# Kernel tuning notes

Hardware: AMD Instinct MI355X
Metric: run time of the kernel (lower is better)

The kernel has to match this reference:

```python
import jax, jax.numpy as jnp
import numpy as np

N, D_IN, H, OUT, L = 6144, 512, 512, 256, 3
EPS = 1e-5


def setup_inputs() -> dict:
    key = jax.random.key(0)
    ks = jax.random.split(key, 32)
    inp = {}
    inp["X"] = jax.random.normal(ks[0], (N, D_IN), dtype=jnp.float32)
    inp["adj"] = jax.random.randint(ks[1], (N, N), 0, 2).astype(jnp.float32)
    inp["adj_glo"] = jax.random.randint(ks[2], (N, N), 0, 2).astype(jnp.float32)
    s = 1.0 / np.sqrt(H)
    # projection + its BN
    inp["Wp"] = jax.random.normal(ks[3], (H, D_IN), dtype=jnp.float32) / np.sqrt(D_IN)
    inp["bp"] = jnp.zeros((H,), jnp.float32)
    inp["gp"] = jnp.ones((H,), jnp.float32)
    inp["betap"] = jnp.zeros((H,), jnp.float32)
    # per-layer params; layers 0,1 output H, layer 2 outputs OUT
    outs = [H, H, OUT]
    for i in range(L):
        o = outs[i]
        k = jax.random.split(ks[4 + i], 6)
        inp[f"Wq{i}"] = jax.random.normal(k[0], (H, H), jnp.float32) * s
        inp[f"Wk{i}"] = jax.random.normal(k[1], (H, H), jnp.float32) * s
        inp[f"Wv{i}"] = jax.random.normal(k[2], (H, H), jnp.float32) * s
        inp[f"Wo{i}"] = jax.random.normal(k[3], (o, H), jnp.float32) * s
        inp[f"bo{i}"] = jnp.zeros((o,), jnp.float32)
        inp[f"g{i}"] = jnp.ones((o,), jnp.float32)
        inp[f"beta{i}"] = jnp.zeros((o,), jnp.float32)
    return inp


def _normalize_adj(a):
    # symmetric GCN normalization D^{-1/2} A D^{-1/2}
    d = a.sum(axis=1)
    dis = jnp.where(d > 0, jax.lax.rsqrt(jnp.maximum(d, 1e-12)), 0.0)
    return a * dis[:, None] * dis[None, :]


def _bn(x, g, b):
    # BatchNorm1d, training mode: batch stats, biased variance
    m = x.mean(axis=0)
    v = x.var(axis=0)
    return g * (x - m) * jax.lax.rsqrt(v + EPS) + b


def _attn(h, adj, Wq, Wk, Wv, Wo, bo):
    Q = h @ Wq.T
    K = h @ Wk.T
    V = h @ Wv.T
    scores = (Q @ K.T) / np.sqrt(H)            # [N, N]
    scores = jnp.where(adj == 0, -jnp.inf, scores)
    attn = jax.nn.softmax(scores, axis=-1)
    return (attn @ V) @ Wo.T + bo


def reference(X, adj, adj_glo, Wp, bp, gp, betap,
              Wq0, Wk0, Wv0, Wo0, bo0, g0, beta0,
              Wq1, Wk1, Wv1, Wo1, bo1, g1, beta1,
              Wq2, Wk2, Wv2, Wo2, bo2, g2, beta2):
    # embedding: normalized global adjacency aggregation + projection + BN
    h = _normalize_adj(adj_glo) @ X
    h = h @ Wp.T + bp
    h = _bn(h, gp, betap)
    embed_features = h
    layers = [
        (Wq0, Wk0, Wv0, Wo0, bo0, g0, beta0),
        (Wq1, Wk1, Wv1, Wo1, bo1, g1, beta1),
        (Wq2, Wk2, Wv2, Wo2, bo2, g2, beta2),
    ]
    for i, (Wq, Wk, Wv, Wo, bo, g, b) in enumerate(layers):
        h_s = h
        h = _attn(h, adj, Wq, Wk, Wv, Wo, bo)
        h = jax.nn.relu(_bn(h, g, b))
        if i != L - 1:
            h = h + h_s
    return h, embed_features
```

## Files before the change

kernel.cpp:

```cpp
#include <hip/hip_runtime.h>
#include <cstdint>

#define NROW 6144
#define HDIM 512
#define DOUT 256
#define NEG_INF (-__builtin_inff())

typedef _Float16 half8 __attribute__((ext_vector_type(8)));
typedef _Float16 half4v __attribute__((ext_vector_type(4)));
typedef float f32x4 __attribute__((ext_vector_type(4)));

#define BARRIER() asm volatile("s_barrier" ::: "memory")
#define LGKM0()   asm volatile("s_waitcnt lgkmcnt(0)" ::: "memory")
#define VMCNT4()  asm volatile("s_waitcnt vmcnt(4)" ::: "memory")
#define VMCNT0()  asm volatile("s_waitcnt vmcnt(0)" ::: "memory")

__device__ __forceinline__ void gld_lds16(void* lds, const void* g) {
  __builtin_amdgcn_global_load_lds(
      (const __attribute__((address_space(1))) void*)g,
      (__attribute__((address_space(3))) void*)lds, 16, 0, 0);
}

__global__ __launch_bounds__(512, 2)
void gemm256(const _Float16* __restrict__ A, int lda,
             const _Float16* __restrict__ B, int ldb,
             _Float16* __restrict__ C, int ldc, int Kc, long MN)
{
  __shared__ _Float16 As[2][256][64];
  __shared__ _Float16 Bs[2][256][64];
  const int tid = threadIdx.x;
  const int wave = tid >> 6, lane = tid & 63;
  const int wr = wave >> 2, wc = wave & 3;

  const int gx = gridDim.x, gy = gridDim.y;
  const int nwg = gx * gy * gridDim.z;
  int lin = (blockIdx.z * gy + blockIdx.y) * gx + blockIdx.x;
  int swz = (nwg % 8 == 0) ? ((lin % 8) * (nwg >> 3) + (lin >> 3)) : lin;
  const int bx = swz % gx, by = (swz / gx) % gy, bz = swz / (gx * gy);
  const int row0 = bx * 256, col0 = by * 256;
  const _Float16* Ab = A + (size_t)row0 * lda + (size_t)bz * Kc;
  const _Float16* Bb = B + (size_t)col0 * ldb + (size_t)bz * Kc;
  const int nt = Kc >> 6;

  const int srow = lane >> 3;
  const int sgr  = (lane & 7) ^ srow;

  auto stageA = [&](int buf, int h, int t) {
    const _Float16* src = Ab + (size_t)(h * 128 + wave * 8 + srow) * lda + t * 64 + sgr * 8;
    gld_lds16(&As[buf][h * 128 + wave * 8][0], src);
    gld_lds16(&As[buf][h * 128 + 64 + wave * 8][0], src + (size_t)64 * lda);
  };
  auto stageB = [&](int buf, int h, int t) {
    const _Float16* src = Bb + (size_t)(h * 128 + wave * 8 + srow) * ldb + t * 64 + sgr * 8;
    gld_lds16(&Bs[buf][h * 128 + wave * 8][0], src);
    gld_lds16(&Bs[buf][h * 128 + 64 + wave * 8][0], src + (size_t)64 * ldb);
  };

  const int fr = lane & 15, sq = lane >> 4, fx = fr & 7;
  half8 af[4][2], bLo[2][2], bHi[2][2];
  f32x4 acc[8][4];
  const f32x4 vzero = {0.f, 0.f, 0.f, 0.f};
  #pragma unroll
  for (int f = 0; f < 8; ++f)
    #pragma unroll
    for (int j = 0; j < 4; ++j)
      acc[f][j] = vzero;

  auto dsA = [&](int buf, int mh) {
    #pragma unroll
    for (int i = 0; i < 4; ++i)
      #pragma unroll
      for (int ks = 0; ks < 2; ++ks)
        af[i][ks] = *(const half8*)&As[buf][wr * 128 + mh * 64 + i * 16 + fr]
                                          [((ks * 4 + sq) ^ fx) * 8];
  };
  auto dsBlo = [&](int buf) {
    #pragma unroll
    for (int jj = 0; jj < 2; ++jj)
      #pragma unroll
      for (int ks = 0; ks < 2; ++ks)
        bLo[jj][ks] = *(const half8*)&Bs[buf][wc * 64 + jj * 16 + fr]
                                            [((ks * 4 + sq) ^ fx) * 8];
  };
  auto dsBhi = [&](int buf) {
    #pragma unroll
    for (int jj = 0; jj < 2; ++jj)
      #pragma unroll
      for (int ks = 0; ks < 2; ++ks)
        bHi[jj][ks] = *(const half8*)&Bs[buf][wc * 64 + 32 + jj * 16 + fr]
                                            [((ks * 4 + sq) ^ fx) * 8];
  };
  auto mQlo = [&](int fb) {
    __builtin_amdgcn_s_setprio(1);
    #pragma unroll
    for (int i = 0; i < 4; ++i)
      #pragma unroll
      for (int jj = 0; jj < 2; ++jj)
        #pragma unroll
        for (int ks = 0; ks < 2; ++ks)
          acc[fb + i][jj] = __builtin_amdgcn_mfma_f32_16x16x32_f16(
              af[i][ks], bLo[jj][ks], acc[fb + i][jj], 0, 0, 0);
    __builtin_amdgcn_s_setprio(0);
  };
  auto mQhi = [&](int fb) {
    __builtin_amdgcn_s_setprio(1);
    #pragma unroll
    for (int i = 0; i < 4; ++i)
      #pragma unroll
      for (int jj = 0; jj < 2; ++jj)
        #pragma unroll
        for (int ks = 0; ks < 2; ++ks)
          acc[fb + i][2 + jj] = __builtin_amdgcn_mfma_f32_16x16x32_f16(
              af[i][ks], bHi[jj][ks], acc[fb + i][2 + jj], 0, 0, 0);
    __builtin_amdgcn_s_setprio(0);
  };

  stageA(0, 0, 0); stageA(0, 1, 0); stageB(0, 0, 0); stageB(0, 1, 0);
  stageB(1, 0, 1); stageB(1, 1, 1);
  VMCNT4();
  BARRIER();

  for (int T = 0; T < nt; T += 2) {
    const bool pipe = (T + 2 < nt);
    dsA(0, 0); dsBlo(0);
    stageA(1, 0, T + 1);
    BARRIER(); LGKM0(); mQlo(0); BARRIER();
    dsBhi(0);
    stageA(1, 1, T + 1);
    BARRIER(); LGKM0(); mQhi(0); BARRIER();
    dsA(0, 1);
    if (pipe) stageB(0, 0, T + 2);
    BARRIER(); LGKM0(); mQhi(4); BARRIER();
    if (pipe) { stageB(0, 1, T + 2); VMCNT4(); } else { VMCNT0(); }
    BARRIER(); mQlo(4); BARRIER();
    dsA(1, 0); dsBlo(1);
    if (pipe) stageA(0, 0, T + 2);
    BARRIER(); LGKM0(); mQlo(0); BARRIER();
    dsBhi(1);
    if (pipe) stageA(0, 1, T + 2);
    BARRIER(); LGKM0(); mQhi(0); BARRIER();
    dsA(1, 1);
    if (pipe) stageB(1, 0, T + 3);
    BARRIER(); LGKM0(); mQhi(4); BARRIER();
    if (pipe) { stageB(1, 1, T + 3); VMCNT4(); } else { VMCNT0(); }
    BARRIER(); mQlo(4); BARRIER();
  }

  _Float16* dst = C + (size_t)bz * MN;
  #pragma unroll
  for (int f = 0; f < 8; ++f)
    #pragma unroll
    for (int j = 0; j < 4; ++j)
      #pragma unroll
      for (int r = 0; r < 4; ++r) {
        int row = row0 + wr * 128 + f * 16 + sq * 4 + r;
        int col = col0 + wc * 64 + j * 16 + fr;
        dst[(size_t)row * ldc + col] = (_Float16)acc[f][j][r];
      }
}

__global__ __launch_bounds__(256)
void gemm_f16(const _Float16* __restrict__ A, int lda,
              const _Float16* __restrict__ B, int ldb,
              float* __restrict__ Cf, _Float16* __restrict__ Ch, int ldc,
              int Kc, _Float16* __restrict__ Pk, long MN)
{
  __shared__ _Float16 As[128][32];
  __shared__ _Float16 Bs[128][32];
  const int tid = threadIdx.x;
  const int wave = tid >> 6, lane = tid & 63;
  const int wr = wave >> 1, wc = wave & 1;
  const int row0 = blockIdx.x * 128, col0 = blockIdx.y * 128;
  const int kbase = blockIdx.z * Kc;

  const int sr = lane >> 2;
  const int sk = ((lane & 3) ^ ((lane >> 3) & 3)) * 8;

  f32x4 acc[4][4];
  const f32x4 vzero = {0.f, 0.f, 0.f, 0.f};
  #pragma unroll
  for (int i = 0; i < 4; ++i)
    #pragma unroll
    for (int j = 0; j < 4; ++j)
      acc[i][j] = vzero;

  const int fr = lane & 15;
  const int fk = (((lane >> 4) ^ ((fr >> 1) & 3))) * 8;

  for (int k0 = kbase; k0 < kbase + Kc; k0 += 32) {
    #pragma unroll
    for (int c = 0; c < 2; ++c) {
      int rbase = c * 64 + wave * 16;
      gld_lds16(&As[rbase][0], A + (size_t)(row0 + rbase + sr) * lda + k0 + sk);
      gld_lds16(&Bs[rbase][0], B + (size_t)(col0 + rbase + sr) * ldb + k0 + sk);
    }
    __syncthreads();
    half8 af[4], bf[4];
    #pragma unroll
    for (int i = 0; i < 4; ++i)
      af[i] = *(const half8*)&As[wr * 64 + i * 16 + fr][fk];
    #pragma unroll
    for (int j = 0; j < 4; ++j)
      bf[j] = *(const half8*)&Bs[wc * 64 + j * 16 + fr][fk];
    #pragma unroll
    for (int i = 0; i < 4; ++i)
      #pragma unroll
      for (int j = 0; j < 4; ++j)
        acc[i][j] = __builtin_amdgcn_mfma_f32_16x16x32_f16(af[i], bf[j], acc[i][j], 0, 0, 0);
    __syncthreads();
  }

  const int lr = (lane >> 4) * 4;
  const int lc = lane & 15;
  if (Pk) {
    _Float16* dst = Pk + (size_t)blockIdx.z * MN;
    #pragma unroll
    for (int i = 0; i < 4; ++i)
      #pragma unroll
      for (int j = 0; j < 4; ++j)
        #pragma unroll
        for (int r = 0; r < 4; ++r) {
          int row = row0 + wr * 64 + i * 16 + lr + r;
          int col = col0 + wc * 64 + j * 16 + lc;
          dst[(size_t)row * ldc + col] = (_Float16)acc[i][j][r];
        }
    return;
  }
  #pragma unroll
  for (int i = 0; i < 4; ++i)
    #pragma unroll
    for (int j = 0; j < 4; ++j)
      #pragma unroll
      for (int r = 0; r < 4; ++r) {
        int row = row0 + wr * 64 + i * 16 + lr + r;
        int col = col0 + wc * 64 + j * 16 + lc;
        float v = acc[i][j][r];
        if (Cf) Cf[(size_t)row * ldc + col] = v;
        if (Ch) Ch[(size_t)row * ldc + col] = (_Float16)v;
      }
}

__global__ __launch_bounds__(256)
void reduce_splitk(const _Float16* __restrict__ Pk, long MN, int S, int cshift,
                   const float* __restrict__ rowscale,
                   float* __restrict__ Yf, _Float16* __restrict__ Yh)
{
  long n4 = MN >> 2;
  for (long i = (long)blockIdx.x * 256 + threadIdx.x; i < n4; i += (long)gridDim.x * 256) {
    float s0 = 0, s1 = 0, s2 = 0, s3 = 0;
    for (int z = 0; z < S; ++z) {
      half4v p = ((const half4v*)(Pk + (size_t)z * MN))[i];
      s0 += (float)p[0]; s1 += (float)p[1]; s2 += (float)p[2]; s3 += (float)p[3];
    }
    if (rowscale) {
      float sc = rowscale[(i * 4) >> cshift];
      s0 *= sc; s1 *= sc; s2 *= sc; s3 *= sc;
    }
    if (Yf) {
      float4 o; o.x = s0; o.y = s1; o.z = s2; o.w = s3;
      ((float4*)Yf)[i] = o;
    }
    if (Yh) {
      half4v o;
      o[0] = (_Float16)s0; o[1] = (_Float16)s1; o[2] = (_Float16)s2; o[3] = (_Float16)s3;
      ((half4v*)Yh)[i] = o;
    }
  }
}

__global__ __launch_bounds__(256)
void degree_convert(const float* __restrict__ A, _Float16* __restrict__ Ah,
                    float* __restrict__ dis)
{
  const int row = blockIdx.x;
  const float* a = A + (size_t)row * NROW;
  _Float16* o = Ah + (size_t)row * NROW;
  float s = 0.f;
  #pragma unroll
  for (int it = 0; it < 6; ++it) {
    int j = it * 1024 + threadIdx.x * 4;
    float4 v = *(const float4*)&a[j];
    s += v.x + v.y + v.z + v.w;
    half4v h;
    h[0] = (_Float16)v.x; h[1] = (_Float16)v.y; h[2] = (_Float16)v.z; h[3] = (_Float16)v.w;
    *(half4v*)&o[j] = h;
  }
  #pragma unroll
  for (int off = 32; off; off >>= 1) s += __shfl_xor(s, off);
  __shared__ float red[4];
  if ((threadIdx.x & 63) == 0) red[threadIdx.x >> 6] = s;
  __syncthreads();
  if (threadIdx.x == 0) {
    float d = red[0] + red[1] + red[2] + red[3];
    dis[row] = (d > 0.f) ? rsqrtf(fmaxf(d, 1e-12f)) : 0.f;
  }
}

__global__ __launch_bounds__(192)
void build_mask(const float* __restrict__ adj, uint32_t* __restrict__ bits)
{
  const int row = blockIdx.x;
  const int w = threadIdx.x;
  const float* a = adj + (size_t)row * NROW + w * 32;
  uint32_t m = 0;
  #pragma unroll
  for (int q = 0; q < 8; ++q) {
    float4 x = *(const float4*)&a[q * 4];
    m |= (x.x != 0.f ? 1u : 0u) << (q * 4 + 0);
    m |= (x.y != 0.f ? 1u : 0u) << (q * 4 + 1);
    m |= (x.z != 0.f ? 1u : 0u) << (q * 4 + 2);
    m |= (x.w != 0.f ? 1u : 0u) << (q * 4 + 3);
  }
  bits[(size_t)row * 192 + w] = m;
}

__global__ __launch_bounds__(256)
void convert_f16(const float* __restrict__ x, _Float16* __restrict__ y, float scale, long n4)
{
  for (long i = (long)blockIdx.x * 256 + threadIdx.x; i < n4; i += (long)gridDim.x * 256) {
    float4 v = ((const float4*)x)[i];
    half4v o;
    o[0] = (_Float16)(v.x * scale);
    o[1] = (_Float16)(v.y * scale);
    o[2] = (_Float16)(v.z * scale);
    o[3] = (_Float16)(v.w * scale);
    ((half4v*)y)[i] = o;
  }
}

__global__ __launch_bounds__(256)
void transpose_scale_f16(const float* __restrict__ src, const float* __restrict__ rowscale,
                         _Float16* __restrict__ dst, int R, int C)
{
  __shared__ _Float16 tile[64][72];
  const int c0 = blockIdx.x * 64, r0 = blockIdx.y * 64;
  const int tx4 = (threadIdx.x & 15) * 4, ty = threadIdx.x >> 4;
  #pragma unroll
  for (int p = 0; p < 4; ++p) {
    int r = p * 16 + ty;
    float4 v = *(const float4*)&src[(size_t)(r0 + r) * C + c0 + tx4];
    float sc = rowscale ? rowscale[r0 + r] : 1.0f;
    tile[tx4 + 0][r] = (_Float16)(v.x * sc);
    tile[tx4 + 1][r] = (_Float16)(v.y * sc);
    tile[tx4 + 2][r] = (_Float16)(v.z * sc);
    tile[tx4 + 3][r] = (_Float16)(v.w * sc);
  }
  __syncthreads();
  #pragma unroll
  for (int p = 0; p < 4; ++p) {
    int c = p * 16 + ty;
    half4v o;
    o[0] = tile[c][tx4 + 0];
    o[1] = tile[c][tx4 + 1];
    o[2] = tile[c][tx4 + 2];
    o[3] = tile[c][tx4 + 3];
    *(half4v*)&dst[(size_t)(c0 + c) * R + r0 + tx4] = o;
  }
}

__global__ __launch_bounds__(256)
void transpose_f16(const _Float16* __restrict__ src, int ld,
                   _Float16* __restrict__ dst, int R, int C)
{
  __shared__ _Float16 tile[64][72];
  const int c0 = blockIdx.x * 64, r0 = blockIdx.y * 64;
  const int tx4 = (threadIdx.x & 15) * 4, ty = threadIdx.x >> 4;
  #pragma unroll
  for (int p = 0; p < 4; ++p) {
    int r = p * 16 + ty;
    half4v v = *(const half4v*)&src[(size_t)(r0 + r) * ld + c0 + tx4];
    tile[tx4 + 0][r] = v[0];
    tile[tx4 + 1][r] = v[1];
    tile[tx4 + 2][r] = v[2];
    tile[tx4 + 3][r] = v[3];
  }
  __syncthreads();
  #pragma unroll
  for (int p = 0; p < 4; ++p) {
    int c = p * 16 + ty;
    half4v o;
    o[0] = tile[c][tx4 + 0];
    o[1] = tile[c][tx4 + 1];
    o[2] = tile[c][tx4 + 2];
    o[3] = tile[c][tx4 + 3];
    *(half4v*)&dst[(size_t)(c0 + c) * R + r0 + tx4] = o;
  }
}

__global__ __launch_bounds__(256)
void softmax_mask16(_Float16* __restrict__ Sf, const uint32_t* __restrict__ bits,
                    float* __restrict__ linv)
{
  const int row = blockIdx.x;
  _Float16* s = Sf + (size_t)row * NROW;
  const uint32_t* b = bits + (size_t)row * 192;
  const int tid = threadIdx.x;
  float v[24];
  float m = NEG_INF;
  #pragma unroll
  for (int it = 0; it < 3; ++it) {
    int j = it * 2048 + tid * 8;
    half8 sv = *(const half8*)&s[j];
    uint32_t w = (b[j >> 5] >> (j & 31)) & 0xffu;
    #pragma unroll
    for (int e = 0; e < 8; ++e) {
      float x = ((w >> e) & 1u) ? (float)sv[e] : NEG_INF;
      v[it * 8 + e] = x;
      m = fmaxf(m, x);
    }
  }
  #pragma unroll
  for (int off = 32; off; off >>= 1) m = fmaxf(m, __shfl_xor(m, off));
  __shared__ float red[4];
  const int lane = tid & 63, wave = tid >> 6;
  if (lane == 0) red[wave] = m;
  __syncthreads();
  m = fmaxf(fmaxf(red[0], red[1]), fmaxf(red[2], red[3]));
  __syncthreads();
  float l = 0.f;
  #pragma unroll
  for (int k = 0; k < 24; ++k) {
    float e = (v[k] == NEG_INF) ? 0.f : __expf(v[k] - m);
    v[k] = e; l += e;
  }
  #pragma unroll
  for (int off = 32; off; off >>= 1) l += __shfl_xor(l, off);
  if (lane == 0) red[wave] = l;
  __syncthreads();
  l = red[0] + red[1] + red[2] + red[3];
  if (tid == 0) linv[row] = (l > 0.f) ? (1.f / l) : 0.f;
  #pragma unroll
  for (int it = 0; it < 3; ++it) {
    int j = it * 2048 + tid * 8;
    half8 o;
    #pragma unroll
    for (int e = 0; e < 8; ++e) o[e] = (_Float16)v[it * 8 + e];
    *(half8*)&s[j] = o;
  }
}

__global__ __launch_bounds__(256)
void bn_partial(const _Float16* __restrict__ X, int C,
                float* __restrict__ psum, float* __restrict__ psq)
{
  const int b = blockIdx.x;
  const int tid = threadIdx.x;
  const _Float16* x = X + (size_t)b * 128 * C;
  float s0 = 0, q0 = 0, s1 = 0, q1 = 0;
  for (int r = 0; r < 128; ++r) {
    float a = (float)x[(size_t)r * C + tid];
    s0 += a; q0 += a * a;
    if (C == 512) {
      float c2 = (float)x[(size_t)r * C + tid + 256];
      s1 += c2; q1 += c2 * c2;
    }
  }
  psum[b * C + tid] = s0; psq[b * C + tid] = q0;
  if (C == 512) { psum[b * C + tid + 256] = s1; psq[b * C + tid + 256] = q1; }
}

__global__ void bn_finalize(const float* __restrict__ psum, const float* __restrict__ psq,
                            int C, const float* __restrict__ g, const float* __restrict__ beta,
                            float* __restrict__ scale, float* __restrict__ shift)
{
  int c = threadIdx.x + blockIdx.x * blockDim.x;
  if (c >= C) return;
  float s = 0, q = 0;
  for (int b = 0; b < 48; ++b) { s += psum[b * C + c]; q += psq[b * C + c]; }
  const float invN = 1.0f / 6144.0f;
  float mean = s * invN;
  float var = q * invN - mean * mean;
  float rstd = rsqrtf(fmaxf(var, 0.f) + 1e-5f);
  float sc = g[c] * rstd;
  scale[c] = sc;
  shift[c] = beta[c] - mean * sc;
}

__global__ __launch_bounds__(256)
void bn_apply(const _Float16* __restrict__ X, const float* __restrict__ scale,
              const float* __restrict__ shift, const _Float16* __restrict__ residual,
              float* __restrict__ Yf, _Float16* __restrict__ Yh,
              int Cmask, long total, int do_relu)
{
  for (long i = (long)blockIdx.x * 256 + threadIdx.x; i < total; i += (long)gridDim.x * 256) {
    int c = (int)(i & Cmask);
    float v = (float)X[i] * scale[c] + shift[c];
    if (do_relu) v = fmaxf(v, 0.f);
    if (residual) v += (float)residual[i];
    if (Yf) Yf[i] = v;
    if (Yh) Yh[i] = (_Float16)v;
  }
}

extern "C" void kernel_launch(void* const* d_in, const int* in_sizes, int n_in,
                              void* d_out, int out_size, void* d_ws, size_t ws_size,
                              hipStream_t stream)
{
  (void)in_sizes; (void)n_in; (void)out_size; (void)ws_size;
  const float* X     = (const float*)d_in[0];
  const float* adj   = (const float*)d_in[1];
  const float* adjg  = (const float*)d_in[2];
  const float* Wp    = (const float*)d_in[3];
  const float* gp    = (const float*)d_in[5];
  const float* betap = (const float*)d_in[6];

  float* out_h     = (float*)d_out;
  float* out_embed = out_h + (size_t)NROW * DOUT;

  char* base = (char*)d_ws;
  size_t off = 0;
  auto alloc = [&](size_t bytes) -> void* {
    void* p = base + off;
    off += (bytes + 255) & ~(size_t)255;
    return p;
  };

  const long MN512 = (long)NROW * 512;

  _Float16* Ag  = (_Float16*)alloc((size_t)NROW * NROW * 2);
  _Float16* Sf  = Ag;
  uint32_t* bits = (uint32_t*)alloc((size_t)NROW * 192 * 4);
  _Float16* Pk  = (_Float16*)alloc((size_t)16 * MN512 * 2);
  _Float16* XsT = (_Float16*)alloc((size_t)HDIM * NROW * 2);
  _Float16* Yh16 = (_Float16*)alloc((size_t)NROW * HDIM * 2);
  _Float16* Wph = (_Float16*)alloc((size_t)HDIM * HDIM * 2);
  _Float16* QKVW[3];
  for (int i = 0; i < 3; ++i) QKVW[i] = (_Float16*)alloc((size_t)1536 * HDIM * 2);
  _Float16* Woh[3];
  Woh[0] = (_Float16*)alloc((size_t)512 * 512 * 2);
  Woh[1] = (_Float16*)alloc((size_t)512 * 512 * 2);
  Woh[2] = (_Float16*)alloc((size_t)256 * 512 * 2);
  _Float16* QKVh = (_Float16*)alloc((size_t)NROW * 1536 * 2);
  _Float16* VTh  = (_Float16*)alloc((size_t)HDIM * NROW * 2);
  _Float16* AVh  = (_Float16*)alloc((size_t)NROW * HDIM * 2);
  _Float16* xh   = (_Float16*)alloc((size_t)NROW * HDIM * 2);
  _Float16* hb16A = (_Float16*)alloc((size_t)NROW * HDIM * 2);
  _Float16* hb16B = (_Float16*)alloc((size_t)NROW * HDIM * 2);
  float* dis  = (float*)alloc((size_t)NROW * 4);
  float* linv = (float*)alloc((size_t)NROW * 4);
  float* psum = (float*)alloc((size_t)48 * 512 * 4);
  float* psq  = (float*)alloc((size_t)48 * 512 * 4);
  float* bnsc = (float*)alloc(512 * 4);
  float* bnsh = (float*)alloc(512 * 4);

  const float qk_scale = 0.21022410381342863f;

  degree_convert<<<NROW, 256, 0, stream>>>(adjg, Ag, dis);
  build_mask<<<NROW, 192, 0, stream>>>(adj, bits);
  transpose_scale_f16<<<dim3(8, 96), 256, 0, stream>>>(X, dis, XsT, NROW, HDIM);
  convert_f16<<<128, 256, 0, stream>>>(Wp, Wph, 1.f, 512 * 512 / 4);
  for (int i = 0; i < 3; ++i) {
    const float* Wq = (const float*)d_in[7 + i * 7 + 0];
    const float* Wk = (const float*)d_in[7 + i * 7 + 1];
    const float* Wv = (const float*)d_in[7 + i * 7 + 2];
    const float* Wo = (const float*)d_in[7 + i * 7 + 3];
    int o = (i < 2) ? 512 : 256;
    convert_f16<<<128, 256, 0, stream>>>(Wq, QKVW[i], qk_scale, 512 * 512 / 4);
    convert_f16<<<128, 256, 0, stream>>>(Wk, QKVW[i] + 512 * 512, qk_scale, 512 * 512 / 4);
    convert_f16<<<128, 256, 0, stream>>>(Wv, QKVW[i] + 2 * 512 * 512, 1.f, 512 * 512 / 4);
    convert_f16<<<128, 256, 0, stream>>>(Wo, Woh[i], 1.f, (long)o * 512 / 4);
  }

  gemm256<<<dim3(24, 2, 16), 512, 0, stream>>>(Ag, NROW, XsT, NROW, Pk, 512, 384, MN512);
  reduce_splitk<<<1536, 256, 0, stream>>>(Pk, MN512, 16, 9, dis, nullptr, Yh16);
  gemm_f16<<<dim3(48, 4), 256, 0, stream>>>(Yh16, HDIM, Wph, HDIM, nullptr, xh, HDIM,
                                            512, nullptr, 0);
  bn_partial<<<48, 256, 0, stream>>>(xh, 512, psum, psq);
  bn_finalize<<<2, 256, 0, stream>>>(psum, psq, 512, gp, betap, bnsc, bnsh);
  bn_apply<<<2048, 256, 0, stream>>>(xh, bnsc, bnsh, nullptr, out_embed, hb16A,
                                     511, MN512, 0);

  _Float16* hbuf[2] = {hb16A, hb16B};
  int cur = 0;
  for (int i = 0; i < 3; ++i) {
    int o = (i < 2) ? 512 : 256;
    const float* gl = (const float*)d_in[7 + i * 7 + 5];
    const float* bl = (const float*)d_in[7 + i * 7 + 6];
    _Float16* hin = hbuf[cur];

    gemm_f16<<<dim3(48, 12), 256, 0, stream>>>(hin, HDIM, QKVW[i], HDIM, nullptr, QKVh, 1536,
                                               512, nullptr, 0);
    transpose_f16<<<dim3(8, 96), 256, 0, stream>>>(QKVh + 1024, 1536, VTh, NROW, HDIM);
    gemm256<<<dim3(24, 24), 512, 0, stream>>>(QKVh, 1536, QKVh + 512, 1536, Sf, NROW, 512, 0);
    softmax_mask16<<<NROW, 256, 0, stream>>>(Sf, bits, linv);
    gemm256<<<dim3(24, 2, 16), 512, 0, stream>>>(Sf, NROW, VTh, NROW, Pk, 512, 384, MN512);
    reduce_splitk<<<1536, 256, 0, stream>>>(Pk, MN512, 16, 9, linv, nullptr, AVh);
    long MNo = (long)NROW * o;
    gemm_f16<<<dim3(48, o / 128, 4), 256, 0, stream>>>(AVh, HDIM, Woh[i], HDIM,
                                                       nullptr, nullptr, o, 128, Pk, MNo);
    reduce_splitk<<<1536, 256, 0, stream>>>(Pk, MNo, 4, (o == 512) ? 9 : 8, nullptr,
                                            nullptr, xh);
    bn_partial<<<48, 256, 0, stream>>>(xh, o, psum, psq);
    bn_finalize<<<2, 256, 0, stream>>>(psum, psq, o, gl, bl, bnsc, bnsh);
    if (i < 2) {
      bn_apply<<<2048, 256, 0, stream>>>(xh, bnsc, bnsh, hin, nullptr, hbuf[cur ^ 1],
                                         o - 1, (long)NROW * o, 1);
      cur ^= 1;
    } else {
      bn_apply<<<2048, 256, 0, stream>>>(xh, bnsc, bnsh, nullptr, out_h, nullptr,
                                         o - 1, (long)NROW * o, 1);
    }
  }
}
```

Baseline: 997.8 us.

## Fuse softmax exponentiation into PV GEMM, batch weight conversions, widen BN partials

```diff
diff --git a/kernel.cpp b/kernel.cpp
--- a/kernel.cpp
+++ b/kernel.cpp
@@ -241,6 +241,91 @@
 }
 
 __global__ __launch_bounds__(256)
+void pv_exp(const _Float16* __restrict__ S, const _Float16* __restrict__ VT,
+            const uint32_t* __restrict__ bits, const float* __restrict__ mrow,
+            _Float16* __restrict__ Pk, int Kc, long MN)
+{
+  __shared__ _Float16 As[128][32];
+  __shared__ _Float16 Bs[128][32];
+  const int tid = threadIdx.x;
+  const int wave = tid >> 6, lane = tid & 63;
+  const int wr = wave >> 1, wc = wave & 1;
+  const int row0 = blockIdx.x * 128, col0 = blockIdx.y * 128;
+  const int kbase = blockIdx.z * Kc;
+
+  const int sr = lane >> 2;
+  const int lsl = (lane & 3) ^ ((lane >> 3) & 3);
+  const int psl = lane & 3;
+
+  int arow[2]; float mv[2]; const uint32_t* brow[2]; size_t sbase[2];
+  #pragma unroll
+  for (int c = 0; c < 2; ++c) {
+    arow[c] = row0 + c * 64 + wave * 16 + sr;
+    mv[c] = mrow[arow[c]];
+    brow[c] = bits + (size_t)arow[c] * 192;
+    sbase[c] = (size_t)arow[c] * NROW + kbase + lsl * 8;
+  }
+
+  f32x4 acc[4][4];
+  const f32x4 vzero = {0.f, 0.f, 0.f, 0.f};
+  #pragma unroll
+  for (int i = 0; i < 4; ++i)
+    #pragma unroll
+    for (int j = 0; j < 4; ++j)
+      acc[i][j] = vzero;
+
+  const int fr = lane & 15;
+  const int fk = (((lane >> 4) ^ ((fr >> 1) & 3))) * 8;
+
+  for (int k0 = 0; k0 < Kc; k0 += 32) {
+    #pragma unroll
+    for (int c = 0; c < 2; ++c) {
+      int rbase = c * 64 + wave * 16;
+      gld_lds16(&Bs[rbase][0], VT + (size_t)(col0 + rbase + sr) * NROW + kbase + k0 + lsl * 8);
+    }
+    #pragma unroll
+    for (int c = 0; c < 2; ++c) {
+      int kv = kbase + k0 + lsl * 8;
+      half8 sv = *(const half8*)&S[sbase[c] + k0];
+      uint32_t w = (brow[c][kv >> 5] >> (kv & 31)) & 0xffu;
+      half8 pvv;
+      #pragma unroll
+      for (int e = 0; e < 8; ++e)
+        pvv[e] = (_Float16)(((w >> e) & 1u) ? __expf((float)sv[e] - mv[c]) : 0.f);
+      *(half8*)&As[c * 64 + wave * 16 + sr][psl * 8] = pvv;
+    }
+    __syncthreads();
+    half8 af[4], bf[4];
+    #pragma unroll
+    for (int i = 0; i < 4; ++i)
+      af[i] = *(const half8*)&As[wr * 64 + i * 16 + fr][fk];
+    #pragma unroll
+    for (int j = 0; j < 4; ++j)
+      bf[j] = *(const half8*)&Bs[wc * 64 + j * 16 + fr][fk];
+    #pragma unroll
+    for (int i = 0; i < 4; ++i)
+      #pragma unroll
+      for (int j = 0; j < 4; ++j)
+        acc[i][j] = __builtin_amdgcn_mfma_f32_16x16x32_f16(af[i], bf[j], acc[i][j], 0, 0, 0);
+    __syncthreads();
+  }
+
+  const int lr = (lane >> 4) * 4;
+  const int lc = lane & 15;
+  _Float16* dst = Pk + (size_t)blockIdx.z * MN;
+  #pragma unroll
+  for (int i = 0; i < 4; ++i)
+    #pragma unroll
+    for (int j = 0; j < 4; ++j)
+      #pragma unroll
+      for (int r = 0; r < 4; ++r) {
+        int row = row0 + wr * 64 + i * 16 + lr + r;
+        int col = col0 + wc * 64 + j * 16 + lc;
+        dst[(size_t)row * 512 + col] = (_Float16)acc[i][j][r];
+      }
+}
+
+__global__ __launch_bounds__(256)
 void reduce_splitk(const _Float16* __restrict__ Pk, long MN, int S, int cshift,
                    const float* __restrict__ rowscale,
                    float* __restrict__ Yf, _Float16* __restrict__ Yh)
@@ -314,16 +399,26 @@
   bits[(size_t)row * 192 + w] = m;
 }
 
-__global__ __launch_bounds__(256)
-void convert_f16(const float* __restrict__ x, _Float16* __restrict__ y, float scale, long n4)
-{
-  for (long i = (long)blockIdx.x * 256 + threadIdx.x; i < n4; i += (long)gridDim.x * 256) {
+struct WConv {
+  const float* src[13];
+  _Float16* dst[13];
+  int n4[13];
+  float scale[13];
+};
+__global__ __launch_bounds__(256)
+void convert_weights(WConv w)
+{
+  const int seg = blockIdx.x >> 4;
+  const int bi = blockIdx.x & 15;
+  const float* x = w.src[seg];
+  _Float16* y = w.dst[seg];
+  const float sc = w.scale[seg];
+  const int n4 = w.n4[seg];
+  for (int i = bi * 256 + threadIdx.x; i < n4; i += 16 * 256) {
     float4 v = ((const float4*)x)[i];
     half4v o;
-    o[0] = (_Float16)(v.x * scale);
-    o[1] = (_Float16)(v.y * scale);
-    o[2] = (_Float16)(v.z * scale);
-    o[3] = (_Float16)(v.w * scale);
+    o[0] = (_Float16)(v.x * sc); o[1] = (_Float16)(v.y * sc);
+    o[2] = (_Float16)(v.z * sc); o[3] = (_Float16)(v.w * sc);
     ((half4v*)y)[i] = o;
   }
 }
@@ -388,11 +483,11 @@
 }
 
 __global__ __launch_bounds__(256)
-void softmax_mask16(_Float16* __restrict__ Sf, const uint32_t* __restrict__ bits,
-                    float* __restrict__ linv)
+void softmax_stats(const _Float16* __restrict__ Sf, const uint32_t* __restrict__ bits,
+                   float* __restrict__ mrow, float* __restrict__ linv)
 {
   const int row = blockIdx.x;
-  _Float16* s = Sf + (size_t)row * NROW;
+  const _Float16* s = Sf + (size_t)row * NROW;
   const uint32_t* b = bits + (size_t)row * 192;
   const int tid = threadIdx.x;
   float v[24];
@@ -419,23 +514,16 @@
   __syncthreads();
   float l = 0.f;
   #pragma unroll
-  for (int k = 0; k < 24; ++k) {
-    float e = (v[k] == NEG_INF) ? 0.f : __expf(v[k] - m);
-    v[k] = e; l += e;
-  }
+  for (int k = 0; k < 24; ++k)
+    l += (v[k] == NEG_INF) ? 0.f : __expf(v[k] - m);
   #pragma unroll
   for (int off = 32; off; off >>= 1) l += __shfl_xor(l, off);
   if (lane == 0) red[wave] = l;
   __syncthreads();
-  l = red[0] + red[1] + red[2] + red[3];
-  if (tid == 0) linv[row] = (l > 0.f) ? (1.f / l) : 0.f;
-  #pragma unroll
-  for (int it = 0; it < 3; ++it) {
-    int j = it * 2048 + tid * 8;
-    half8 o;
-    #pragma unroll
-    for (int e = 0; e < 8; ++e) o[e] = (_Float16)v[it * 8 + e];
-    *(half8*)&s[j] = o;
+  if (tid == 0) {
+    l = red[0] + red[1] + red[2] + red[3];
+    mrow[row] = m;
+    linv[row] = (l > 0.f) ? (1.f / l) : 0.f;
   }
 }
 
@@ -444,19 +532,35 @@
                 float* __restrict__ psum, float* __restrict__ psq)
 {
   const int b = blockIdx.x;
-  const int tid = threadIdx.x;
-  const _Float16* x = X + (size_t)b * 128 * C;
-  float s0 = 0, q0 = 0, s1 = 0, q1 = 0;
-  for (int r = 0; r < 128; ++r) {
-    float a = (float)x[(size_t)r * C + tid];
-    s0 += a; q0 += a * a;
-    if (C == 512) {
-      float c2 = (float)x[(size_t)r * C + tid + 256];
-      s1 += c2; q1 += c2 * c2;
-    }
-  }
-  psum[b * C + tid] = s0; psq[b * C + tid] = q0;
-  if (C == 512) { psum[b * C + tid + 256] = s1; psq[b * C + tid + 256] = q1; }
+  const int t = threadIdx.x;
+  const int tpc = C >> 3;
+  const int ng = 256 / tpc;
+  const int g = t / tpc, c8 = (t % tpc) * 8;
+  const int rpg = 64 / ng;
+  const _Float16* x = X + (size_t)b * 64 * C;
+  float s[8], q[8];
+  #pragma unroll
+  for (int e = 0; e < 8; ++e) { s[e] = 0.f; q[e] = 0.f; }
+  for (int r = g * rpg; r < (g + 1) * rpg; ++r) {
+    half8 v = *(const half8*)&x[(size_t)r * C + c8];
+    #pragma unroll
+    for (int e = 0; e < 8; ++e) {
+      float f = (float)v[e];
+      s[e] += f; q[e] += f * f;
+    }
+  }
+  __shared__ float ls[256][8], lq[256][8];
+  #pragma unroll
+  for (int e = 0; e < 8; ++e) { ls[t][e] = s[e]; lq[t][e] = q[e]; }
+  __syncthreads();
+  for (int u = t; u < C; u += 256) {
+    float ss = 0, qq = 0;
+    for (int gg = 0; gg < ng; ++gg) {
+      ss += ls[gg * tpc + (u >> 3)][u & 7];
+      qq += lq[gg * tpc + (u >> 3)][u & 7];
+    }
+    psum[b * C + u] = ss; psq[b * C + u] = qq;
+  }
 }
 
 __global__ void bn_finalize(const float* __restrict__ psum, const float* __restrict__ psq,
@@ -466,7 +570,7 @@
   int c = threadIdx.x + blockIdx.x * blockDim.x;
   if (c >= C) return;
   float s = 0, q = 0;
-  for (int b = 0; b < 48; ++b) { s += psum[b * C + c]; q += psq[b * C + c]; }
+  for (int b = 0; b < 96; ++b) { s += psum[b * C + c]; q += psq[b * C + c]; }
   const float invN = 1.0f / 6144.0f;
   float mean = s * invN;
   float var = q * invN - mean * mean;
@@ -520,7 +624,7 @@
   _Float16* Ag  = (_Float16*)alloc((size_t)NROW * NROW * 2);
   _Float16* Sf  = Ag;
   uint32_t* bits = (uint32_t*)alloc((size_t)NROW * 192 * 4);
-  _Float16* Pk  = (_Float16*)alloc((size_t)16 * MN512 * 2);
+  _Float16* Pk  = (_Float16*)alloc((size_t)8 * MN512 * 2);
   _Float16* XsT = (_Float16*)alloc((size_t)HDIM * NROW * 2);
   _Float16* Yh16 = (_Float16*)alloc((size_t)NROW * HDIM * 2);
   _Float16* Wph = (_Float16*)alloc((size_t)HDIM * HDIM * 2);
@@ -537,9 +641,10 @@
   _Float16* hb16A = (_Float16*)alloc((size_t)NROW * HDIM * 2);
   _Float16* hb16B = (_Float16*)alloc((size_t)NROW * HDIM * 2);
   float* dis  = (float*)alloc((size_t)NROW * 4);
+  float* mrow = (float*)alloc((size_t)NROW * 4);
   float* linv = (float*)alloc((size_t)NROW * 4);
-  float* psum = (float*)alloc((size_t)48 * 512 * 4);
-  float* psq  = (float*)alloc((size_t)48 * 512 * 4);
+  float* psum = (float*)alloc((size_t)96 * 512 * 4);
+  float* psq  = (float*)alloc((size_t)96 * 512 * 4);
   float* bnsc = (float*)alloc(512 * 4);
   float* bnsh = (float*)alloc(512 * 4);
 
@@ -548,24 +653,30 @@
   degree_convert<<<NROW, 256, 0, stream>>>(adjg, Ag, dis);
   build_mask<<<NROW, 192, 0, stream>>>(adj, bits);
   transpose_scale_f16<<<dim3(8, 96), 256, 0, stream>>>(X, dis, XsT, NROW, HDIM);
-  convert_f16<<<128, 256, 0, stream>>>(Wp, Wph, 1.f, 512 * 512 / 4);
-  for (int i = 0; i < 3; ++i) {
-    const float* Wq = (const float*)d_in[7 + i * 7 + 0];
-    const float* Wk = (const float*)d_in[7 + i * 7 + 1];
-    const float* Wv = (const float*)d_in[7 + i * 7 + 2];
-    const float* Wo = (const float*)d_in[7 + i * 7 + 3];
-    int o = (i < 2) ? 512 : 256;
-    convert_f16<<<128, 256, 0, stream>>>(Wq, QKVW[i], qk_scale, 512 * 512 / 4);
-    convert_f16<<<128, 256, 0, stream>>>(Wk, QKVW[i] + 512 * 512, qk_scale, 512 * 512 / 4);
-    convert_f16<<<128, 256, 0, stream>>>(Wv, QKVW[i] + 2 * 512 * 512, 1.f, 512 * 512 / 4);
-    convert_f16<<<128, 256, 0, stream>>>(Wo, Woh[i], 1.f, (long)o * 512 / 4);
-  }
-
-  gemm256<<<dim3(24, 2, 16), 512, 0, stream>>>(Ag, NROW, XsT, NROW, Pk, 512, 384, MN512);
-  reduce_splitk<<<1536, 256, 0, stream>>>(Pk, MN512, 16, 9, dis, nullptr, Yh16);
+
+  {
+    WConv w;
+    int seg = 0;
+    w.src[seg] = Wp; w.dst[seg] = Wph; w.n4[seg] = 512 * 512 / 4; w.scale[seg] = 1.f; ++seg;
+    for (int i = 0; i < 3; ++i) {
+      int o = (i < 2) ? 512 : 256;
+      w.src[seg] = (const float*)d_in[7 + i * 7 + 0]; w.dst[seg] = QKVW[i];
+      w.n4[seg] = 512 * 512 / 4; w.scale[seg] = qk_scale; ++seg;
+      w.src[seg] = (const float*)d_in[7 + i * 7 + 1]; w.dst[seg] = QKVW[i] + 512 * 512;
+      w.n4[seg] = 512 * 512 / 4; w.scale[seg] = qk_scale; ++seg;
+      w.src[seg] = (const float*)d_in[7 + i * 7 + 2]; w.dst[seg] = QKVW[i] + 2 * 512 * 512;
+      w.n4[seg] = 512 * 512 / 4; w.scale[seg] = 1.f; ++seg;
+      w.src[seg] = (const float*)d_in[7 + i * 7 + 3]; w.dst[seg] = Woh[i];
+      w.n4[seg] = o * 512 / 4; w.scale[seg] = 1.f; ++seg;
+    }
+    convert_weights<<<13 * 16, 256, 0, stream>>>(w);
+  }
+
+  gemm256<<<dim3(24, 2, 8), 512, 0, stream>>>(Ag, NROW, XsT, NROW, Pk, 512, 768, MN512);
+  reduce_splitk<<<1536, 256, 0, stream>>>(Pk, MN512, 8, 9, dis, nullptr, Yh16);
   gemm_f16<<<dim3(48, 4), 256, 0, stream>>>(Yh16, HDIM, Wph, HDIM, nullptr, xh, HDIM,
                                             512, nullptr, 0);
-  bn_partial<<<48, 256, 0, stream>>>(xh, 512, psum, psq);
+  bn_partial<<<96, 256, 0, stream>>>(xh, 512, psum, psq);
   bn_finalize<<<2, 256, 0, stream>>>(psum, psq, 512, gp, betap, bnsc, bnsh);
   bn_apply<<<2048, 256, 0, stream>>>(xh, bnsc, bnsh, nullptr, out_embed, hb16A,
                                      511, MN512, 0);
@@ -582,15 +693,15 @@
                                                512, nullptr, 0);
     transpose_f16<<<dim3(8, 96), 256, 0, stream>>>(QKVh + 1024, 1536, VTh, NROW, HDIM);
     gemm256<<<dim3(24, 24), 512, 0, stream>>>(QKVh, 1536, QKVh + 512, 1536, Sf, NROW, 512, 0);
-    softmax_mask16<<<NROW, 256, 0, stream>>>(Sf, bits, linv);
-    gemm256<<<dim3(24, 2, 16), 512, 0, stream>>>(Sf, NROW, VTh, NROW, Pk, 512, 384, MN512);
-    reduce_splitk<<<1536, 256, 0, stream>>>(Pk, MN512, 16, 9, linv, nullptr, AVh);
+    softmax_stats<<<NROW, 256, 0, stream>>>(Sf, bits, mrow, linv);
+    pv_exp<<<dim3(48, 4, 8), 256, 0, stream>>>(Sf, VTh, bits, mrow, Pk, 768, MN512);
+    reduce_splitk<<<1536, 256, 0, stream>>>(Pk, MN512, 8, 9, linv, nullptr, AVh);
     long MNo = (long)NROW * o;
     gemm_f16<<<dim3(48, o / 128, 4), 256, 0, stream>>>(AVh, HDIM, Woh[i], HDIM,
                                                        nullptr, nullptr, o, 128, Pk, MNo);
     reduce_splitk<<<1536, 256, 0, stream>>>(Pk, MNo, 4, (o == 512) ? 9 : 8, nullptr,
                                             nullptr, xh);
-    bn_partial<<<48, 256, 0, stream>>>(xh, o, psum, psq);
+    bn_partial<<<96, 256, 0, stream>>>(xh, o, psum, psq);
     bn_finalize<<<2, 256, 0, stream>>>(psum, psq, o, gl, bl, bnsc, bnsh);
     if (i < 2) {
       bn_apply<<<2048, 256, 0, stream>>>(xh, bnsc, bnsh, hin, nullptr, hbuf[cur ^ 1],
```

Result: faster. 901.2 us (-9.7%).
